# Kernel optimization log

Measured on AMD Instinct MI355X. Metric: run time of the kernel, lower is better.

The kernel has to match this reference:

```python
import jax, jax.numpy as jnp
import numpy as np

B = 2048
GIN = 128      # gating input features
GH = 128       # gating hidden units
E = 8          # experts
XIN = 512      # expert input features
U = 512        # expert layer units
OUT = 512      # expert output features


def setup_inputs() -> dict:
    key = jax.random.key(0)
    ks = jax.random.split(key, 16)
    rn = lambda k, shape: (jax.random.normal(k, shape) * 0.05).astype(jnp.float32)
    return {
        "gating_input": jax.random.normal(ks[0], (B, GIN), dtype=jnp.float32),
        "expert_input": jax.random.normal(ks[1], (B, XIN), dtype=jnp.float32),
        # gating MLP params (Dense stores kernel as (in, out))
        "Wg0": rn(ks[2], (GIN, GH)), "bg0": rn(ks[3], (GH,)),
        "Wg1": rn(ks[4], (GH, GH)), "bg1": rn(ks[5], (GH,)),
        "Wgo": rn(ks[6], (GH, E)),  "bgo": rn(ks[7], (E,)),
        # expert weight pools: alpha (E, units, in), beta (E, units)
        "alpha0": rn(ks[8], (E, U, XIN)), "beta0": rn(ks[9], (E, U)),
        "alpha1": rn(ks[10], (E, U, U)),  "beta1": rn(ks[11], (E, U)),
        "alpha2": rn(ks[12], (E, OUT, U)), "beta2": rn(ks[13], (E, OUT)),
    }


def dense_expert(x, g, alpha, beta):
    # Mathematically: (sum_e g[b,e] * alpha[e]) @ x[b] + sum_e g[b,e]*beta[e]
    # Contract input with each expert first (avoids the (B,U,I) blended-weight tensor).
    per_expert = jnp.einsum("bi,eui->beu", x, alpha)   # (B, E, U)
    w = jnp.einsum("be,beu->bu", g, per_expert)         # (B, U)
    b = jnp.einsum("be,eu->bu", g, beta)                # (B, U)
    return w + b


def reference(gating_input, expert_input, Wg0, bg0, Wg1, bg1, Wgo, bgo,
              alpha0, beta0, alpha1, beta1, alpha2, beta2):
    # Gating network: Dense+ELU x2 (dropout is identity at inference), Dense+softmax
    h = jax.nn.elu(gating_input @ Wg0 + bg0)
    h = jax.nn.elu(h @ Wg1 + bg1)
    g = jax.nn.softmax(h @ Wgo + bgo, axis=-1)          # (B, E)

    # Expert network: DenseExpert + ELU x2, final DenseExpert
    x = jax.nn.elu(dense_expert(expert_input, g, alpha0, beta0))
    x = jax.nn.elu(dense_expert(x, g, alpha1, beta1))
    y = dense_expert(x, g, alpha2, beta2)               # (B, OUT)
    return y
```

## Files before the change

kernel.cpp:

```cpp
#include <hip/hip_runtime.h>
#include <math.h>

#define BATCH 2048
#define GIN 128
#define GH 128
#define NE 8
#define XIN 512
#define UU 512

typedef __attribute__((ext_vector_type(8))) short short8;
typedef __attribute__((ext_vector_type(4))) float f32x4;

#define AS1 __attribute__((address_space(1)))
#define AS3 __attribute__((address_space(3)))

__device__ inline unsigned short f2bf(float f) {
    unsigned u = __float_as_uint(f);
    u += 0x7fffu + ((u >> 16) & 1u);
    return (unsigned short)(u >> 16);
}

__device__ inline float elu1(float x) { return x > 0.f ? x : (expf(x) - 1.f); }

__global__ __launch_bounds__(256) void pre_kernel(
    const float* __restrict__ gin, const float* __restrict__ W0, const float* __restrict__ b0,
    const float* __restrict__ W1, const float* __restrict__ b1,
    const float* __restrict__ Wo, const float* __restrict__ bo,
    float* __restrict__ g,
    const float* __restrict__ a0, const float* __restrict__ a1, const float* __restrict__ a2,
    const float* __restrict__ xv, unsigned short* __restrict__ dst)
{
    __shared__ float xs[4][128];
    __shared__ float hs[4][128];
    __shared__ float ps[2][4][128];
    __shared__ float lp[8][4][8];
    __shared__ float ls[4][8];

    const int t = threadIdx.x;

    if (blockIdx.x >= 512) {
        const long long vi = ((long long)(blockIdx.x - 512) * 256 + t) * 4;
        const int sel = (int)(vi >> 21);
        const float* src = (sel == 0) ? a0 : (sel == 1) ? a1 : (sel == 2) ? a2 : xv;
        float4 v = *(const float4*)(src + (vi & ((1 << 21) - 1)));
        union { unsigned short us[4]; uint2 u2; } p;
        p.us[0] = f2bf(v.x); p.us[1] = f2bf(v.y); p.us[2] = f2bf(v.z); p.us[3] = f2bf(v.w);
        *(uint2*)(dst + vi) = p.u2;
        return;
    }

    const int c = t & 127;
    const int h = t >> 7;
    const int row0 = blockIdx.x * 4;

    ((float*)xs)[t]       = gin[row0 * GIN + t];
    ((float*)xs)[t + 256] = gin[row0 * GIN + t + 256];
    __syncthreads();

    {
        float acc0 = 0.f, acc1 = 0.f, acc2 = 0.f, acc3 = 0.f;
        const float* Wc = W0 + c;
        #pragma unroll 8
        for (int i = h * 64; i < h * 64 + 64; ++i) {
            float w = Wc[i * GH];
            acc0 += xs[0][i] * w; acc1 += xs[1][i] * w;
            acc2 += xs[2][i] * w; acc3 += xs[3][i] * w;
        }
        ps[h][0][c] = acc0; ps[h][1][c] = acc1; ps[h][2][c] = acc2; ps[h][3][c] = acc3;
    }
    __syncthreads();
    {
        int o = t, r = o >> 7, cc = o & 127;
        hs[r][cc] = elu1(ps[0][r][cc] + ps[1][r][cc] + b0[cc]);
        o = t + 256; r = o >> 7; cc = o & 127;
        hs[r][cc] = elu1(ps[0][r][cc] + ps[1][r][cc] + b0[cc]);
    }
    __syncthreads();

    {
        float acc0 = 0.f, acc1 = 0.f, acc2 = 0.f, acc3 = 0.f;
        const float* Wc = W1 + c;
        #pragma unroll 8
        for (int i = h * 64; i < h * 64 + 64; ++i) {
            float w = Wc[i * GH];
            acc0 += hs[0][i] * w; acc1 += hs[1][i] * w;
            acc2 += hs[2][i] * w; acc3 += hs[3][i] * w;
        }
        ps[h][0][c] = acc0; ps[h][1][c] = acc1; ps[h][2][c] = acc2; ps[h][3][c] = acc3;
    }
    __syncthreads();
    {
        int o = t, r = o >> 7, cc = o & 127;
        xs[r][cc] = elu1(ps[0][r][cc] + ps[1][r][cc] + b1[cc]);
        o = t + 256; r = o >> 7; cc = o & 127;
        xs[r][cc] = elu1(ps[0][r][cc] + ps[1][r][cc] + b1[cc]);
    }
    __syncthreads();

    {
        const int e = t & 7, r = (t >> 3) & 3, q = t >> 5;
        float s = 0.f;
        #pragma unroll
        for (int i = q * 16; i < q * 16 + 16; ++i) s += xs[r][i] * Wo[i * NE + e];
        lp[q][r][e] = s;
    }
    __syncthreads();
    if (t < 32) {
        const int r = t >> 3, e = t & 7;
        float s = bo[e];
        #pragma unroll
        for (int q = 0; q < 8; ++q) s += lp[q][r][e];
        ls[r][e] = s;
    }
    __syncthreads();
    if (t < 4) {
        float mx = ls[t][0];
        #pragma unroll
        for (int e = 1; e < 8; ++e) mx = fmaxf(mx, ls[t][e]);
        float s = 0.f, ex[8];
        #pragma unroll
        for (int e = 0; e < 8; ++e) { ex[e] = expf(ls[t][e] - mx); s += ex[e]; }
        float inv = 1.f / s;
        #pragma unroll
        for (int e = 0; e < 8; ++e) g[(row0 + t) * NE + e] = ex[e] * inv;
    }
}

__global__ __launch_bounds__(256) void moe_layer_kernel(
    const unsigned short* __restrict__ A,
    const unsigned short* __restrict__ Bw,
    const float* __restrict__ g,
    const float* __restrict__ beta,
    unsigned short* __restrict__ Xnext,
    float* __restrict__ out, int last)
{
    constexpr int K = XIN;
    __shared__ unsigned short As[3][64 * 32];
    __shared__ float red[4][64][32];
    __shared__ float gs[64][8];
    __shared__ float bt[8][32];

    const int t = threadIdx.x;
    const int bid = blockIdx.x;
    const int n0 = (bid & 15) * 32;
    const int m0 = (bid >> 4) * 64;
    const int wave = t >> 6, lane = t & 63;
    const int e0 = 2 * wave;

    ((float2*)gs)[t] = ((const float2*)(g + (size_t)m0 * NE))[t];
    bt[t >> 5][t & 31] = beta[(t >> 5) * UU + n0 + (t & 31)];

    f32x4 acc[2][4][2] = {};

    const int slot = t & 3;
    const int arow = t >> 2;
    const int acol = ((slot ^ ((arow >> 1) & 3)) * 8);
    const unsigned short* a_src = A + (size_t)(m0 + arow) * K + acol;

    const int fr = lane & 15;
    const int kq = (lane >> 4) * 8;
    const unsigned short* b_ptr[2][2];
    #pragma unroll
    for (int ep = 0; ep < 2; ++ep)
        #pragma unroll
        for (int j = 0; j < 2; ++j)
            b_ptr[ep][j] = Bw + ((size_t)(e0 + ep) * UU + n0 + j * 16 + fr) * K + kq;

#define STAGE_A(bi, ki)                                                      \
    __builtin_amdgcn_global_load_lds(                                        \
        (const AS1 void*)(a_src + (ki)),                                     \
        (AS3 void*)(&As[bi][t * 8]), 16, 0, 0)

#define LOADB(dst, ki)                                                       \
    do {                                                                     \
        dst[0] = *(const short8*)(b_ptr[0][0] + (ki));                       \
        dst[1] = *(const short8*)(b_ptr[0][1] + (ki));                       \
        dst[2] = *(const short8*)(b_ptr[1][0] + (ki));                       \
        dst[3] = *(const short8*)(b_ptr[1][1] + (ki));                       \
    } while (0)

#define COMPUTE(bi, bf)                                                      \
    do {                                                                     \
        const int fkb_ = (lane >> 4) * 16;                                   \
        const char* Ab_ = (const char*)(&As[bi][0]);                         \
        short8 af_[4];                                                       \
        _Pragma("unroll")                                                    \
        for (int i = 0; i < 4; ++i) {                                        \
            const int row_ = fr + i * 16;                                    \
            af_[i] = *(const short8*)(Ab_ +                                  \
                     ((row_ * 64 + fkb_) ^ (((row_ >> 1) & 3) << 4)));       \
        }                                                                    \
        _Pragma("unroll")                                                    \
        for (int ep = 0; ep < 2; ++ep)                                       \
            _Pragma("unroll")                                                \
            for (int i = 0; i < 4; ++i)                                      \
                _Pragma("unroll")                                            \
                for (int j = 0; j < 2; ++j)                                  \
                    acc[ep][i][j] = __builtin_amdgcn_mfma_f32_16x16x32_bf16( \
                        af_[i], bf[ep * 2 + j], acc[ep][i][j], 0, 0, 0);     \
    } while (0)

    short8 bb0[4], bb1[4], bb2[4];

    STAGE_A(0, 0);  LOADB(bb0, 0);
    STAGE_A(1, 32); LOADB(bb1, 32);
    asm volatile("s_waitcnt vmcnt(5)" ::: "memory");
    __builtin_amdgcn_s_barrier();

    #pragma unroll
    for (int s = 0; s < 16; ++s) {
        const int cur = s % 3;
        if (cur == 0)      COMPUTE(0, bb0);
        else if (cur == 1) COMPUTE(1, bb1);
        else               COMPUTE(2, bb2);

        if (s + 2 < 16) {
            const int pre = (s + 2) % 3;
            STAGE_A(pre, (s + 2) * 32);
            if (pre == 0)      LOADB(bb0, (s + 2) * 32);
            else if (pre == 1) LOADB(bb1, (s + 2) * 32);
            else               LOADB(bb2, (s + 2) * 32);
        }
        if (s < 15) {
            if (s + 2 < 16) asm volatile("s_waitcnt vmcnt(5)" ::: "memory");
            else            asm volatile("s_waitcnt vmcnt(0)" ::: "memory");
            __builtin_amdgcn_s_barrier();
        }
    }

    const int cl = lane & 15, rq = lane >> 4;
    #pragma unroll
    for (int i = 0; i < 4; ++i)
        #pragma unroll
        for (int j = 0; j < 2; ++j)
            #pragma unroll
            for (int r = 0; r < 4; ++r) {
                const int rl = i * 16 + rq * 4 + r;
                const int co = j * 16 + cl;
                const float v =
                    gs[rl][e0]     * (acc[0][i][j][r] + bt[e0][co]) +
                    gs[rl][e0 + 1] * (acc[1][i][j][r] + bt[e0 + 1][co]);
                red[wave][rl][co] = v;
            }
    __syncthreads();

    {
        const int rl = t >> 2;
        const int c0 = (t & 3) * 8;
        float v[8];
        #pragma unroll
        for (int u = 0; u < 8; ++u)
            v[u] = red[0][rl][c0 + u] + red[1][rl][c0 + u] +
                   red[2][rl][c0 + u] + red[3][rl][c0 + u];
        if (last) {
            float4 o0 = {v[0], v[1], v[2], v[3]};
            float4 o1 = {v[4], v[5], v[6], v[7]};
            float* op = out + (size_t)(m0 + rl) * UU + n0 + c0;
            *(float4*)op = o0;
            *(float4*)(op + 4) = o1;
        } else {
            union { unsigned short us[8]; short8 s8; } p;
            #pragma unroll
            for (int u = 0; u < 8; ++u) p.us[u] = f2bf(elu1(v[u]));
            *(short8*)(Xnext + (size_t)(m0 + rl) * UU + n0 + c0) = p.s8;
        }
    }
#undef STAGE_A
#undef LOADB
#undef COMPUTE
}

extern "C" void kernel_launch(void* const* d_in, const int* in_sizes, int n_in,
                              void* d_out, int out_size, void* d_ws, size_t ws_size,
                              hipStream_t stream)
{
    (void)in_sizes; (void)n_in; (void)out_size; (void)ws_size;
    const float* gin = (const float*)d_in[0];
    const float* xin = (const float*)d_in[1];
    const float* W0  = (const float*)d_in[2];
    const float* b0  = (const float*)d_in[3];
    const float* W1  = (const float*)d_in[4];
    const float* b1  = (const float*)d_in[5];
    const float* Wo  = (const float*)d_in[6];
    const float* bo  = (const float*)d_in[7];
    const float* alpha[3] = {(const float*)d_in[8],  (const float*)d_in[10], (const float*)d_in[12]};
    const float* beta[3]  = {(const float*)d_in[9],  (const float*)d_in[11], (const float*)d_in[13]};
    float* out = (float*)d_out;

    char* ws = (char*)d_ws;
    float* g = (float*)ws;
    size_t off = 65536;
    unsigned short* ab = (unsigned short*)(ws + off);
    off += (size_t)3 * (1 << 21) * 2;
    unsigned short* Xb0 = (unsigned short*)(ws + off);
    off += (size_t)BATCH * XIN * 2;
    unsigned short* Xb1 = (unsigned short*)(ws + off);
    off += (size_t)BATCH * XIN * 2;

    pre_kernel<<<512 + 7168, 256, 0, stream>>>(
        gin, W0, b0, W1, b1, Wo, bo, g,
        alpha[0], alpha[1], alpha[2], xin, ab);

    unsigned short* Xsrc = Xb0;
    unsigned short* Xdst = Xb1;
    for (int l = 0; l < 3; ++l) {
        moe_layer_kernel<<<512, 256, 0, stream>>>(
            Xsrc, ab + (size_t)l * (1 << 21), g, beta[l], Xdst, out, l == 2 ? 1 : 0);
        unsigned short* tmp = Xsrc; Xsrc = Xdst; Xdst = tmp;
    }
}
```

Before: 160.4 us.

## Fuse three MoE layer launches into one persistent kernel with grid barriers

Replaces the three per-layer GEMM launches with a single persistent kernel of 512 blocks that loops over the layers. It synchronises the whole grid between layers with an atomic counter and generation barrier. The goal is to remove two kernel launch gaps and the associated tail drain. In exchange it depends on all 512 blocks being co-resident (launch_bounds 2 blocks per CU on 256 CUs), and the spin barrier has a timeout that could silently break correctness.

```diff
diff --git a/kernel.cpp b/kernel.cpp
--- a/kernel.cpp
+++ b/kernel.cpp
@@ -22,13 +22,37 @@
 
 __device__ inline float elu1(float x) { return x > 0.f ? x : (expf(x) - 1.f); }
 
+__device__ __forceinline__ void grid_barrier(unsigned* bar, unsigned nb)
+{
+    __syncthreads();
+    if (threadIdx.x == 0) {
+        unsigned* cnt = bar;
+        unsigned* gen = bar + 1;
+        const unsigned g0 = __hip_atomic_load(gen, __ATOMIC_RELAXED, __HIP_MEMORY_SCOPE_AGENT);
+        const unsigned prev = __hip_atomic_fetch_add(cnt, 1u, __ATOMIC_ACQ_REL, __HIP_MEMORY_SCOPE_AGENT);
+        if (prev == nb - 1) {
+            __hip_atomic_store(cnt, 0u, __ATOMIC_RELAXED, __HIP_MEMORY_SCOPE_AGENT);
+            __hip_atomic_fetch_add(gen, 1u, __ATOMIC_RELEASE, __HIP_MEMORY_SCOPE_AGENT);
+        } else {
+            int spins = 0;
+            while (__hip_atomic_load(gen, __ATOMIC_ACQUIRE, __HIP_MEMORY_SCOPE_AGENT) == g0) {
+                __builtin_amdgcn_s_sleep(2);
+                if (++spins > (1 << 22)) break;
+            }
+        }
+    }
+    __threadfence();
+    __syncthreads();
+}
+
 __global__ __launch_bounds__(256) void pre_kernel(
     const float* __restrict__ gin, const float* __restrict__ W0, const float* __restrict__ b0,
     const float* __restrict__ W1, const float* __restrict__ b1,
     const float* __restrict__ Wo, const float* __restrict__ bo,
     float* __restrict__ g,
     const float* __restrict__ a0, const float* __restrict__ a1, const float* __restrict__ a2,
-    const float* __restrict__ xv, unsigned short* __restrict__ dst)
+    const float* __restrict__ xv, unsigned short* __restrict__ dst,
+    unsigned* __restrict__ bar)
 {
     __shared__ float xs[4][128];
     __shared__ float hs[4][128];
@@ -37,6 +61,8 @@
     __shared__ float ls[4][8];
 
     const int t = threadIdx.x;
+
+    if (blockIdx.x == 0 && t == 0) { bar[0] = 0u; bar[1] = 0u; }
 
     if (blockIdx.x >= 512) {
         const long long vi = ((long long)(blockIdx.x - 512) * 256 + t) * 4;
@@ -126,13 +152,14 @@
     }
 }
 
-__global__ __launch_bounds__(256) void moe_layer_kernel(
-    const unsigned short* __restrict__ A,
-    const unsigned short* __restrict__ Bw,
+__global__ __launch_bounds__(256, 2) void moe_persistent_kernel(
+    const unsigned short* __restrict__ ab,
     const float* __restrict__ g,
-    const float* __restrict__ beta,
-    unsigned short* __restrict__ Xnext,
-    float* __restrict__ out, int last)
+    const float* __restrict__ be0, const float* __restrict__ be1,
+    const float* __restrict__ be2,
+    unsigned short* __restrict__ Xb0, unsigned short* __restrict__ Xb1,
+    float* __restrict__ out,
+    unsigned* __restrict__ bar)
 {
     constexpr int K = XIN;
     __shared__ unsigned short As[3][64 * 32];
@@ -146,25 +173,33 @@
     const int m0 = (bid >> 4) * 64;
     const int wave = t >> 6, lane = t & 63;
     const int e0 = 2 * wave;
-
-    ((float2*)gs)[t] = ((const float2*)(g + (size_t)m0 * NE))[t];
-    bt[t >> 5][t & 31] = beta[(t >> 5) * UU + n0 + (t & 31)];
-
-    f32x4 acc[2][4][2] = {};
-
+    const int fr = lane & 15;
+    const int kq = (lane >> 4) * 8;
     const int slot = t & 3;
     const int arow = t >> 2;
     const int acol = ((slot ^ ((arow >> 1) & 3)) * 8);
-    const unsigned short* a_src = A + (size_t)(m0 + arow) * K + acol;
-
-    const int fr = lane & 15;
-    const int kq = (lane >> 4) * 8;
-    const unsigned short* b_ptr[2][2];
-    #pragma unroll
-    for (int ep = 0; ep < 2; ++ep)
-        #pragma unroll
-        for (int j = 0; j < 2; ++j)
-            b_ptr[ep][j] = Bw + ((size_t)(e0 + ep) * UU + n0 + j * 16 + fr) * K + kq;
+    const int cl = lane & 15, rq = lane >> 4;
+
+    ((float2*)gs)[t] = ((const float2*)(g + (size_t)m0 * NE))[t];
+
+    for (int l = 0; l < 3; ++l) {
+        const unsigned short* A  = (l == 1) ? Xb1 : Xb0;
+        unsigned short* Xnext    = (l == 0) ? Xb1 : Xb0;
+        const unsigned short* Bw = ab + (size_t)l * (1 << 21);
+        const float* beta = (l == 0) ? be0 : (l == 1) ? be1 : be2;
+        const int last = (l == 2);
+
+        bt[t >> 5][t & 31] = beta[(t >> 5) * UU + n0 + (t & 31)];
+
+        f32x4 acc[2][4][2] = {};
+
+        const unsigned short* a_src = A + (size_t)(m0 + arow) * K + acol;
+        const unsigned short* b_ptr[2][2];
+        #pragma unroll
+        for (int ep = 0; ep < 2; ++ep)
+            #pragma unroll
+            for (int j = 0; j < 2; ++j)
+                b_ptr[ep][j] = Bw + ((size_t)(e0 + ep) * UU + n0 + j * 16 + fr) * K + kq;
 
 #define STAGE_A(bi, ki)                                                      \
     __builtin_amdgcn_global_load_lds(                                        \
@@ -200,74 +235,76 @@
                         af_[i], bf[ep * 2 + j], acc[ep][i][j], 0, 0, 0);     \
     } while (0)
 
-    short8 bb0[4], bb1[4], bb2[4];
-
-    STAGE_A(0, 0);  LOADB(bb0, 0);
-    STAGE_A(1, 32); LOADB(bb1, 32);
-    asm volatile("s_waitcnt vmcnt(5)" ::: "memory");
-    __builtin_amdgcn_s_barrier();
-
-    #pragma unroll
-    for (int s = 0; s < 16; ++s) {
-        const int cur = s % 3;
-        if (cur == 0)      COMPUTE(0, bb0);
-        else if (cur == 1) COMPUTE(1, bb1);
-        else               COMPUTE(2, bb2);
-
-        if (s + 2 < 16) {
-            const int pre = (s + 2) % 3;
-            STAGE_A(pre, (s + 2) * 32);
-            if (pre == 0)      LOADB(bb0, (s + 2) * 32);
-            else if (pre == 1) LOADB(bb1, (s + 2) * 32);
-            else               LOADB(bb2, (s + 2) * 32);
-        }
-        if (s < 15) {
-            if (s + 2 < 16) asm volatile("s_waitcnt vmcnt(5)" ::: "memory");
-            else            asm volatile("s_waitcnt vmcnt(0)" ::: "memory");
-            __builtin_amdgcn_s_barrier();
-        }
-    }
-
-    const int cl = lane & 15, rq = lane >> 4;
-    #pragma unroll
-    for (int i = 0; i < 4; ++i)
-        #pragma unroll
-        for (int j = 0; j < 2; ++j)
+        short8 bb0[4], bb1[4], bb2[4];
+
+        STAGE_A(0, 0);  LOADB(bb0, 0);
+        STAGE_A(1, 32); LOADB(bb1, 32);
+        asm volatile("s_waitcnt vmcnt(5)" ::: "memory");
+        __builtin_amdgcn_s_barrier();
+
+        #pragma unroll
+        for (int s = 0; s < 16; ++s) {
+            const int cur = s % 3;
+            if (cur == 0)      COMPUTE(0, bb0);
+            else if (cur == 1) COMPUTE(1, bb1);
+            else               COMPUTE(2, bb2);
+
+            if (s + 2 < 16) {
+                const int pre = (s + 2) % 3;
+                STAGE_A(pre, (s + 2) * 32);
+                if (pre == 0)      LOADB(bb0, (s + 2) * 32);
+                else if (pre == 1) LOADB(bb1, (s + 2) * 32);
+                else               LOADB(bb2, (s + 2) * 32);
+            }
+            if (s < 15) {
+                if (s + 2 < 16) asm volatile("s_waitcnt vmcnt(5)" ::: "memory");
+                else            asm volatile("s_waitcnt vmcnt(0)" ::: "memory");
+                __builtin_amdgcn_s_barrier();
+            }
+        }
+
+        #pragma unroll
+        for (int i = 0; i < 4; ++i)
             #pragma unroll
-            for (int r = 0; r < 4; ++r) {
-                const int rl = i * 16 + rq * 4 + r;
-                const int co = j * 16 + cl;
-                const float v =
-                    gs[rl][e0]     * (acc[0][i][j][r] + bt[e0][co]) +
-                    gs[rl][e0 + 1] * (acc[1][i][j][r] + bt[e0 + 1][co]);
-                red[wave][rl][co] = v;
+            for (int j = 0; j < 2; ++j)
+                #pragma unroll
+                for (int r = 0; r < 4; ++r) {
+                    const int rl = i * 16 + rq * 4 + r;
+                    const int co = j * 16 + cl;
+                    const float v =
+                        gs[rl][e0]     * (acc[0][i][j][r] + bt[e0][co]) +
+                        gs[rl][e0 + 1] * (acc[1][i][j][r] + bt[e0 + 1][co]);
+                    red[wave][rl][co] = v;
+                }
+        __syncthreads();
+
+        {
+            const int rl = t >> 2;
+            const int c0 = (t & 3) * 8;
+            float v[8];
+            #pragma unroll
+            for (int u = 0; u < 8; ++u)
+                v[u] = red[0][rl][c0 + u] + red[1][rl][c0 + u] +
+                       red[2][rl][c0 + u] + red[3][rl][c0 + u];
+            if (last) {
+                float4 o0 = {v[0], v[1], v[2], v[3]};
+                float4 o1 = {v[4], v[5], v[6], v[7]};
+                float* op = out + (size_t)(m0 + rl) * UU + n0 + c0;
+                *(float4*)op = o0;
+                *(float4*)(op + 4) = o1;
+            } else {
+                union { unsigned short us[8]; short8 s8; } p;
+                #pragma unroll
+                for (int u = 0; u < 8; ++u) p.us[u] = f2bf(elu1(v[u]));
+                *(short8*)(Xnext + (size_t)(m0 + rl) * UU + n0 + c0) = p.s8;
             }
-    __syncthreads();
-
-    {
-        const int rl = t >> 2;
-        const int c0 = (t & 3) * 8;
-        float v[8];
-        #pragma unroll
-        for (int u = 0; u < 8; ++u)
-            v[u] = red[0][rl][c0 + u] + red[1][rl][c0 + u] +
-                   red[2][rl][c0 + u] + red[3][rl][c0 + u];
-        if (last) {
-            float4 o0 = {v[0], v[1], v[2], v[3]};
-            float4 o1 = {v[4], v[5], v[6], v[7]};
-            float* op = out + (size_t)(m0 + rl) * UU + n0 + c0;
-            *(float4*)op = o0;
-            *(float4*)(op + 4) = o1;
-        } else {
-            union { unsigned short us[8]; short8 s8; } p;
-            #pragma unroll
-            for (int u = 0; u < 8; ++u) p.us[u] = f2bf(elu1(v[u]));
-            *(short8*)(Xnext + (size_t)(m0 + rl) * UU + n0 + c0) = p.s8;
-        }
-    }
+        }
+
+        if (l < 2) grid_barrier(bar, gridDim.x);
 #undef STAGE_A
 #undef LOADB
 #undef COMPUTE
+    }
 }
 
 extern "C" void kernel_launch(void* const* d_in, const int* in_sizes, int n_in,
@@ -284,7 +321,9 @@
     const float* Wo  = (const float*)d_in[6];
     const float* bo  = (const float*)d_in[7];
     const float* alpha[3] = {(const float*)d_in[8],  (const float*)d_in[10], (const float*)d_in[12]};
-    const float* beta[3]  = {(const float*)d_in[9],  (const float*)d_in[11], (const float*)d_in[13]};
+    const float* be0 = (const float*)d_in[9];
+    const float* be1 = (const float*)d_in[11];
+    const float* be2 = (const float*)d_in[13];
     float* out = (float*)d_out;
 
     char* ws = (char*)d_ws;
@@ -296,16 +335,13 @@
     off += (size_t)BATCH * XIN * 2;
     unsigned short* Xb1 = (unsigned short*)(ws + off);
     off += (size_t)BATCH * XIN * 2;
+    unsigned* bar = (unsigned*)(ws + off);
+    off += 64;
 
     pre_kernel<<<512 + 7168, 256, 0, stream>>>(
         gin, W0, b0, W1, b1, Wo, bo, g,
-        alpha[0], alpha[1], alpha[2], xin, ab);
-
-    unsigned short* Xsrc = Xb0;
-    unsigned short* Xdst = Xb1;
-    for (int l = 0; l < 3; ++l) {
-        moe_layer_kernel<<<512, 256, 0, stream>>>(
-            Xsrc, ab + (size_t)l * (1 << 21), g, beta[l], Xdst, out, l == 2 ? 1 : 0);
-        unsigned short* tmp = Xsrc; Xsrc = Xdst; Xdst = tmp;
-    }
-}
+        alpha[0], alpha[1], alpha[2], xin, ab, bar);
+
+    moe_persistent_kernel<<<512, 256, 0, stream>>>(
+        ab, g, be0, be1, be2, Xb0, Xb1, out, bar);
+}
```

Result: slower. 312.7 us (+95.0%).
